# Optimization experiments

Hardware: AMD Instinct MI355X
Metric: run time of the kernel (lower is better)

## Reference

```python
import jax, jax.numpy as jnp
import numpy as np

TEMP = 1.0
EULER_GAMMA = 0.5772156649015329
BIG = 1.0e9


def setup_inputs() -> dict:
    key = jax.random.key(0)
    k = jax.random.split(key, 8)
    B, N, D, H = 32, 1024, 1024, 512  # batch, seq, d_model, hidden_size//2
    queries = jax.random.normal(k[0], (B, N, D), jnp.float32)
    queries_mask = jnp.ones((B, N), dtype=bool)
    W1 = jax.random.normal(k[1], (D, H), jnp.float32) * 0.02
    b1 = jnp.zeros((H,), jnp.float32)
    W2 = jax.random.normal(k[2], (H, 1), jnp.float32) * 0.02
    b2 = jnp.zeros((1,), jnp.float32)
    uniform_noise = jax.random.uniform(k[3], (B, N, 1), jnp.float32, 0.0, 1e-5)
    gumbel_noise = jax.random.gumbel(k[4], (B, N, 1), jnp.float32)
    return {"queries": queries, "queries_mask": queries_mask, "W1": W1, "b1": b1,
            "W2": W2, "b2": b2, "uniform_noise": uniform_noise,
            "gumbel_noise": gumbel_noise, "action_refinement": 1}


def reference(queries, queries_mask, W1, b1, W2, b2, uniform_noise, gumbel_noise, action_refinement):
    B, N, D = queries.shape
    # block0: Dense(H, relu) -> Dense(1); then softplus clamp + log + tiny uniform noise
    h = jax.nn.relu(jnp.einsum('bnd,dh->bnh', queries, W1) + b1)
    acts = jnp.einsum('bnh,ho->bno', h, W2) + b2                      # [B,N,1]
    acts = jnp.log(jnp.maximum(jax.nn.softplus(acts), 1e-5)) + uniform_noise
    acts = jnp.repeat(acts, action_refinement, axis=0)                # [BR,N,1]
    vmask = jnp.repeat(queries_mask[:, None, :].astype(jnp.float32), action_refinement, axis=0)  # [BR,1,N]
    n_valid = jnp.sum(vmask, axis=-1)                                 # [BR,1]
    mask_n1 = jnp.transpose(vmask, (0, 2, 1))                         # [BR,N,1]
    sqz_mask = mask_n1[..., 0]                                        # [BR,N]
    masked_acts = jnp.where(mask_n1 > 0, acts, -1e6)                  # [BR,N,1]
    perturb = masked_acts + gumbel_noise                              # [BR,N,1]
    # deterministic NeuralSort
    s = (jnp.exp(perturb) * mask_n1)[..., 0]                          # [BR,N]
    A = jnp.abs(s[:, :, None] - s[:, None, :])                        # [BR,N,N]
    Bmat = jnp.sum(A, axis=-1, keepdims=True)                         # A @ (1 1^T): row sums broadcast
    scaling = (N + 1 - 2 * (jnp.arange(N) + 1)).astype(jnp.float32)   # [N]
    C = s[:, :, None] * scaling[None, None, :]                        # [BR,N,N]
    P_hat = jnp.transpose(C - Bmat, (0, 2, 1)) - (1.0 - vmask) * BIG  # [BR,N,N]
    # greedy argmax permutation extraction (find_permu), vectorized over batch
    BR = P_hat.shape[0]
    def step(flag, row):                                              # row: [BR,N]
        tmp = row - flag * BIG
        idx = jnp.argmax(tmp, axis=-1)
        flag = jnp.maximum(flag, jax.nn.one_hot(idx, N, dtype=flag.dtype))
        return flag, idx
    _, idxs = jax.lax.scan(step, jnp.zeros((BR, N), jnp.float32), jnp.transpose(P_hat, (1, 0, 2)))
    chosen = jnp.transpose(idxs).astype(jnp.int32)                    # [BR,N]
    chosen = jnp.concatenate([jnp.zeros((BR, 1), jnp.int32), chosen[:, :-1]], axis=-1)
    id_permu = jnp.arange(N, dtype=jnp.int32)[None, :]
    permu = jnp.where(sqz_mask > 0, chosen, id_permu)                 # [BR,N]
    sample_permu = jax.nn.one_hot(permu, N, axis=-1, dtype=jnp.float32)
    # Plackett-Luce log-likelihood of sampled permutation
    exp_actis = jnp.exp(jnp.take_along_axis(masked_acts[..., 0], permu, axis=-1))
    rev_cumsum = jnp.cumsum(exp_actis[:, ::-1], axis=-1)[:, ::-1]
    eps = 1e-20
    log_nom = (jnp.log(exp_actis + eps) - jnp.log(rev_cumsum + eps)) * sqz_mask
    log_nom = jnp.sum(log_nom, axis=-1, keepdims=True)                # [BR,1]
    log_norm = jnp.zeros_like(log_nom)
    # KL term
    sqz_acts = acts[..., 0]
    kl1 = n_valid * (np.log(TEMP) - 1.0 + EULER_GAMMA * (1.0 / TEMP - 1.0))
    s1 = (1.0 / TEMP) * jnp.sum(sqz_acts * sqz_mask, axis=-1).reshape(-1, 1)
    s2 = jnp.sum(jnp.exp(-1.0 / TEMP * jnp.maximum(sqz_acts * sqz_mask, -20.0 * TEMP)), axis=-1).reshape(-1, 1) - (jnp.float32(N) - n_valid)
    kl = kl1 + s1 + s2 * jnp.exp(jax.lax.lgamma(jnp.float32(1.0 + 1.0 / TEMP)))
    return sample_permu, masked_acts[..., 0], kl, log_nom, log_norm
```

## Files before the change

### kernel.cpp

```cpp
#include <hip/hip_runtime.h>
#include <math.h>

#define BB 32
#define NN 1024
#define DD 1024
#define HH 512

#define OUT0_OFF 0
#define OUT1_OFF (BB * NN * NN)
#define OUT2_OFF (OUT1_OFF + BB * NN)
#define OUT3_OFF (OUT2_OFF + BB)
#define OUT4_OFF (OUT3_OFF + BB)

#define WS_ACTS 0
#define WS_W1T  131072
#define WS_RANK 1179648

typedef __attribute__((ext_vector_type(8))) short short8;
typedef __attribute__((ext_vector_type(4))) float floatx4;

__device__ inline unsigned int f2bf(float x) {
    unsigned int u = __builtin_bit_cast(unsigned int, x);
    return (u + 0x7FFFu + ((u >> 16) & 1u)) >> 16;
}

__device__ inline void gload_lds16(const void* g, void* l) {
    __builtin_amdgcn_global_load_lds(
        (const __attribute__((address_space(1))) unsigned int*)g,
        (__attribute__((address_space(3))) unsigned int*)l, 16, 0, 0);
}

__global__ __launch_bounds__(1024) void w1t_kernel(const float* __restrict__ W1,
                                                   unsigned short* __restrict__ W1T)
{
    __shared__ float T[32][33];
    const int tx = threadIdx.x, ty = threadIdx.y;
    const int d0 = blockIdx.x * 32, h0 = blockIdx.y * 32;
    T[ty][tx] = W1[(d0 + ty) * HH + h0 + tx];
    __syncthreads();
    W1T[(size_t)(h0 + ty) * DD + d0 + tx] = (unsigned short)f2bf(T[tx][ty]);
}

#define MT 128
__global__ __launch_bounds__(512, 2) void gemm_acts_kernel(
    const float* __restrict__ q, const unsigned short* __restrict__ W1T,
    const float* __restrict__ b1, const float* __restrict__ W2,
    const float* __restrict__ b2, const float* __restrict__ unoise,
    float* __restrict__ acts_ws, float* __restrict__ out1)
{
    __shared__ short As[2][MT * 32];
    __shared__ short Bs[2][HH * 32];
    __shared__ float red[MT][4];

    const int tid  = threadIdx.x;
    const int w    = tid >> 6;
    const int lane = tid & 63;
    const int c    = lane & 15;
    const int qd   = lane >> 4;
    const int wr   = (w >> 2) * 64;
    const int wc   = (w & 3) * 128;
    const int m0   = blockIdx.x * MT;

    floatx4 acc[8][4];
    #pragma unroll
    for (int tn = 0; tn < 8; ++tn)
        #pragma unroll
        for (int tm = 0; tm < 4; ++tm)
            acc[tn][tm] = (floatx4){0.f, 0.f, 0.f, 0.f};

    int boff[4];
    #pragma unroll
    for (int j = 0; j < 4; ++j) {
        int n  = (w * 4 + j) * 16 + (lane >> 2);
        int c0 = (lane & 3) * 16;
        int s  = (n >> 1) & 3;
        boff[j] = n * 2048 + (c0 ^ (s << 4));
    }
    const char* w1tb = (const char*)W1T;

    const int srow = tid >> 2, skp = tid & 3;
    const float* aptr = q + (size_t)(m0 + srow) * DD + skp * 8;
    const int asw = (skp * 16) ^ (((srow >> 1) & 3) << 4);

    int aoff[4], boffr[8];
    #pragma unroll
    for (int tm = 0; tm < 4; ++tm) {
        int r = wr + tm * 16 + c;
        aoff[tm] = r * 64 + ((qd * 16) ^ (((r >> 1) & 3) << 4));
    }
    #pragma unroll
    for (int tn = 0; tn < 8; ++tn) {
        int n = wc + tn * 16 + c;
        boffr[tn] = n * 64 + ((qd * 16) ^ (((n >> 1) & 3) << 4));
    }

    float4 a0, a1;

    #pragma unroll
    for (int j = 0; j < 4; ++j)
        gload_lds16(w1tb + boff[j], (char*)(&Bs[0][0]) + (w * 4 + j) * 1024);
    {
        const float4* ap = (const float4*)aptr;
        float4 v0 = ap[0], v1 = ap[1];
        uint4 pk;
        pk.x = f2bf(v0.x) | (f2bf(v0.y) << 16);
        pk.y = f2bf(v0.z) | (f2bf(v0.w) << 16);
        pk.z = f2bf(v1.x) | (f2bf(v1.y) << 16);
        pk.w = f2bf(v1.z) | (f2bf(v1.w) << 16);
        *(uint4*)((char*)(&As[0][0]) + srow * 64 + asw) = pk;
        const float4* ap1 = (const float4*)(aptr + 32);
        a0 = ap1[0]; a1 = ap1[1];
    }

    #pragma unroll 1
    for (int kk = 0; kk < 32; ++kk) {
        asm volatile("s_waitcnt vmcnt(0) lgkmcnt(0)" ::: "memory");
        __builtin_amdgcn_s_barrier();

        const int cur = kk & 1, nxt = cur ^ 1;
        if (kk < 31) {
            #pragma unroll
            for (int j = 0; j < 4; ++j)
                gload_lds16(w1tb + (boff[j] + (kk + 1) * 64),
                            (char*)(&Bs[nxt][0]) + (w * 4 + j) * 1024);
            uint4 pk;
            pk.x = f2bf(a0.x) | (f2bf(a0.y) << 16);
            pk.y = f2bf(a0.z) | (f2bf(a0.w) << 16);
            pk.z = f2bf(a1.x) | (f2bf(a1.y) << 16);
            pk.w = f2bf(a1.z) | (f2bf(a1.w) << 16);
            *(uint4*)((char*)(&As[nxt][0]) + srow * 64 + asw) = pk;
            const int ka = (kk < 30) ? kk + 2 : 31;
            const float4* ap = (const float4*)(aptr + ka * 32);
            a0 = ap[0]; a1 = ap[1];
        }
        __builtin_amdgcn_s_setprio(1);
        short8 af[4];
        #pragma unroll
        for (int tm = 0; tm < 4; ++tm)
            af[tm] = *(const short8*)((const char*)(&As[cur][0]) + aoff[tm]);
        #pragma unroll
        for (int tn = 0; tn < 8; ++tn) {
            short8 bf = *(const short8*)((const char*)(&Bs[cur][0]) + boffr[tn]);
            #pragma unroll
            for (int tm = 0; tm < 4; ++tm)
                acc[tn][tm] = __builtin_amdgcn_mfma_f32_16x16x32_bf16(
                    af[tm], bf, acc[tn][tm], 0, 0, 0);
        }
        __builtin_amdgcn_s_setprio(0);
    }

    float b1v[8], w2v[8];
    #pragma unroll
    for (int tn = 0; tn < 8; ++tn) {
        int col = wc + tn * 16 + c;
        b1v[tn] = b1[col];
        w2v[tn] = W2[col];
    }
    #pragma unroll
    for (int tm = 0; tm < 4; ++tm) {
        #pragma unroll
        for (int r = 0; r < 4; ++r) {
            float p = 0.f;
            #pragma unroll
            for (int tn = 0; tn < 8; ++tn) {
                float v = acc[tn][tm][r] + b1v[tn];
                p = fmaf(fmaxf(v, 0.f), w2v[tn], p);
            }
            p += __shfl_xor(p, 1);
            p += __shfl_xor(p, 2);
            p += __shfl_xor(p, 4);
            p += __shfl_xor(p, 8);
            if (c == 0) red[wr + tm * 16 + qd * 4 + r][w & 3] = p;
        }
    }
    __syncthreads();
    if (tid < MT) {
        float raw = red[tid][0] + red[tid][1] + red[tid][2] + red[tid][3] + b2[0];
        float sp = fmaxf(raw, 0.f) + log1pf(expf(-fabsf(raw)));
        int row = m0 + tid;
        float av = logf(fmaxf(sp, 1e-5f)) + unoise[row];
        acts_ws[row] = av;
        out1[row]    = av;
    }
}

__global__ __launch_bounds__(256) void zero_kernel(float4* __restrict__ p, int n4)
{
    int idx = blockIdx.x * blockDim.x + threadIdx.x;
    int stride = gridDim.x * blockDim.x;
    float4 z = make_float4(0.f, 0.f, 0.f, 0.f);
    for (int i = idx; i < n4; i += stride) p[i] = z;
}

__global__ __launch_bounds__(256) void rank_kernel(
    const float* __restrict__ acts_ws, const float* __restrict__ gumbel,
    int* __restrict__ rank)
{
    __shared__ float P[NN];
    const int b = blockIdx.x >> 2;
    const int chunk = blockIdx.x & 3;
    const int tid = threadIdx.x;
    #pragma unroll
    for (int r = 0; r < 4; ++r) {
        int j = r * 256 + tid;
        P[j] = acts_ws[b * NN + j] + gumbel[b * NN + j];
    }
    __syncthreads();
    const int i = chunk * 256 + tid;
    const float pert = P[i];
    int cnt = 0;
    const float4* P4 = (const float4*)P;
    for (int j4 = 0; j4 < NN / 4; ++j4) {
        float4 pv = P4[j4];
        int j = j4 * 4;
        cnt += (pv.x > pert) || (pv.x == pert && j + 0 < i);
        cnt += (pv.y > pert) || (pv.y == pert && j + 1 < i);
        cnt += (pv.z > pert) || (pv.z == pert && j + 2 < i);
        cnt += (pv.w > pert) || (pv.w == pert && j + 3 < i);
    }
    rank[b * NN + i] = cnt;
}

__global__ __launch_bounds__(1024) void permu_stats_kernel(
    const float* __restrict__ acts_ws, const int* __restrict__ rank,
    float* __restrict__ out0, float* __restrict__ out2,
    float* __restrict__ out3, float* __restrict__ out4)
{
    __shared__ float A[NN];
    __shared__ int   IDX[NN];
    __shared__ float WT[16];
    __shared__ float WSUF[17];
    __shared__ float P0[16], P1[16], P2[16];

    const int b = blockIdx.x;
    const int i = threadIdx.x;
    const int lane = i & 63;
    const int w = i >> 6;

    float a = acts_ws[b * NN + i];
    A[i] = a;
    IDX[rank[b * NN + i]] = i;
    __syncthreads();

    int perm = (i == 0) ? 0 : IDX[i - 1];
    out0[((size_t)b * NN + i) * NN + perm] = 1.0f;

    float e = expf(A[perm]);
    float s = e;
    #pragma unroll
    for (int off = 1; off < 64; off <<= 1) {
        float v = __shfl_down(s, off);
        if (lane + off < 64) s += v;
    }
    if (lane == 0) WT[w] = s;
    __syncthreads();
    if (w == 0) {
        float t = (lane < 16) ? WT[lane] : 0.f;
        #pragma unroll
        for (int off = 1; off < 16; off <<= 1) {
            float v = __shfl_down(t, off);
            if (lane + off < 16) t += v;
        }
        if (lane < 16) WSUF[lane] = t;
        if (lane == 0) WSUF[16] = 0.f;
    }
    __syncthreads();

    float S = s + WSUF[w + 1];
    float term = logf(e + 1e-20f) - logf(S + 1e-20f);

    float r0 = term, r1 = a, r2 = expf(-fmaxf(a, -20.f));
    #pragma unroll
    for (int off = 1; off < 64; off <<= 1) {
        r0 += __shfl_xor(r0, off);
        r1 += __shfl_xor(r1, off);
        r2 += __shfl_xor(r2, off);
    }
    if (lane == 0) { P0[w] = r0; P1[w] = r1; P2[w] = r2; }
    __syncthreads();
    if (i == 0) {
        float t0 = 0.f, t1 = 0.f, t2 = 0.f;
        #pragma unroll
        for (int k = 0; k < 16; ++k) { t0 += P0[k]; t1 += P1[k]; t2 += P2[k]; }
        out3[b] = t0;
        out2[b] = -(float)NN + t1 + t2;
        out4[b] = 0.f;
    }
}

extern "C" void kernel_launch(void* const* d_in, const int* in_sizes, int n_in,
                              void* d_out, int out_size, void* d_ws, size_t ws_size,
                              hipStream_t stream)
{
    const float* q      = (const float*)d_in[0];
    const float* W1     = (const float*)d_in[2];
    const float* b1     = (const float*)d_in[3];
    const float* W2     = (const float*)d_in[4];
    const float* b2     = (const float*)d_in[5];
    const float* unoise = (const float*)d_in[6];
    const float* gumbel = (const float*)d_in[7];

    float* out  = (float*)d_out;
    char*  ws   = (char*)d_ws;
    float*          acts = (float*)(ws + WS_ACTS);
    unsigned short* W1T  = (unsigned short*)(ws + WS_W1T);
    int*            rank = (int*)(ws + WS_RANK);

    w1t_kernel<<<dim3(32, 16), dim3(32, 32), 0, stream>>>(W1, W1T);
    gemm_acts_kernel<<<(BB * NN) / MT, 512, 0, stream>>>(q, W1T, b1, W2, b2,
                                                         unoise, acts,
                                                         out + OUT1_OFF);
    zero_kernel<<<8192, 256, 0, stream>>>((float4*)(out + OUT0_OFF),
                                          (BB * NN * NN) / 4);
    rank_kernel<<<BB * 4, 256, 0, stream>>>(acts, gumbel, rank);
    permu_stats_kernel<<<BB, 1024, 0, stream>>>(acts, rank,
                                                out + OUT0_OFF, out + OUT2_OFF,
                                                out + OUT3_OFF, out + OUT4_OFF);
}
```

Measured before the change: 310.9 us.

## Restructure GEMM to 64-row tiles with fine-grained vmcnt pipelining and 4 blocks/CU

Result: slower. 320.4 us (+3.0%).

```diff
diff --git a/kernel.cpp b/kernel.cpp
--- a/kernel.cpp
+++ b/kernel.cpp
@@ -41,29 +41,28 @@
     W1T[(size_t)(h0 + ty) * DD + d0 + tx] = (unsigned short)f2bf(T[tx][ty]);
 }
 
-#define MT 128
-__global__ __launch_bounds__(512, 2) void gemm_acts_kernel(
+#define MT 64
+#define SB() __builtin_amdgcn_sched_barrier(0)
+
+__global__ __launch_bounds__(512, 4) void gemm_acts_kernel(
     const float* __restrict__ q, const unsigned short* __restrict__ W1T,
     const float* __restrict__ b1, const float* __restrict__ W2,
     const float* __restrict__ b2, const float* __restrict__ unoise,
     float* __restrict__ acts_ws, float* __restrict__ out1)
 {
-    __shared__ short As[2][MT * 32];
+    __shared__ short As[2][MT * 64];
     __shared__ short Bs[2][HH * 32];
-    __shared__ float red[MT][4];
 
     const int tid  = threadIdx.x;
     const int w    = tid >> 6;
     const int lane = tid & 63;
     const int c    = lane & 15;
     const int qd   = lane >> 4;
-    const int wr   = (w >> 2) * 64;
-    const int wc   = (w & 3) * 128;
     const int m0   = blockIdx.x * MT;
 
-    floatx4 acc[8][4];
-    #pragma unroll
-    for (int tn = 0; tn < 8; ++tn)
+    floatx4 acc[4][4];
+    #pragma unroll
+    for (int tn = 0; tn < 4; ++tn)
         #pragma unroll
         for (int tm = 0; tm < 4; ++tm)
             acc[tn][tm] = (floatx4){0.f, 0.f, 0.f, 0.f};
@@ -78,91 +77,142 @@
     }
     const char* w1tb = (const char*)W1T;
 
-    const int srow = tid >> 2, skp = tid & 3;
-    const float* aptr = q + (size_t)(m0 + srow) * DD + skp * 8;
-    const int asw = (skp * 16) ^ (((srow >> 1) & 3) << 4);
-
-    int aoff[4], boffr[8];
+    const int arow = tid >> 3;
+    const int agrp = tid & 7;
+    const float* aptrA = q + (size_t)(m0 + arow) * DD + ((agrp ^ (arow & 7)) * 8);
+    const int adst = arow * 128 + agrp * 16;
+
+    int aoffA[4], aoffB[4], boffr[4];
     #pragma unroll
     for (int tm = 0; tm < 4; ++tm) {
-        int r = wr + tm * 16 + c;
-        aoff[tm] = r * 64 + ((qd * 16) ^ (((r >> 1) & 3) << 4));
-    }
-    #pragma unroll
-    for (int tn = 0; tn < 8; ++tn) {
-        int n = wc + tn * 16 + c;
+        int r = tm * 16 + c;
+        aoffA[tm] = r * 128 + 16 * ((qd)     ^ (r & 7));
+        aoffB[tm] = r * 128 + 16 * ((4 + qd) ^ (r & 7));
+    }
+    #pragma unroll
+    for (int tn = 0; tn < 4; ++tn) {
+        int n = w * 64 + tn * 16 + c;
         boffr[tn] = n * 64 + ((qd * 16) ^ (((n >> 1) & 3) << 4));
     }
 
     float4 a0, a1;
 
-    #pragma unroll
-    for (int j = 0; j < 4; ++j)
-        gload_lds16(w1tb + boff[j], (char*)(&Bs[0][0]) + (w * 4 + j) * 1024);
     {
-        const float4* ap = (const float4*)aptr;
-        float4 v0 = ap[0], v1 = ap[1];
+        float4 v0 = *(const float4*)(aptrA + 0);
+        float4 v1 = *(const float4*)(aptrA + 4);
         uint4 pk;
         pk.x = f2bf(v0.x) | (f2bf(v0.y) << 16);
         pk.y = f2bf(v0.z) | (f2bf(v0.w) << 16);
         pk.z = f2bf(v1.x) | (f2bf(v1.y) << 16);
         pk.w = f2bf(v1.z) | (f2bf(v1.w) << 16);
-        *(uint4*)((char*)(&As[0][0]) + srow * 64 + asw) = pk;
-        const float4* ap1 = (const float4*)(aptr + 32);
-        a0 = ap1[0]; a1 = ap1[1];
-    }
+        *(uint4*)((char*)(&As[0][0]) + adst) = pk;
+    }
+    SB();
+    #pragma unroll
+    for (int j = 0; j < 4; ++j)
+        gload_lds16(w1tb + boff[j], (char*)(&Bs[0][0]) + (w * 4 + j) * 1024);
+    SB();
+    a0 = *(const float4*)(aptrA + 64);
+    a1 = *(const float4*)(aptrA + 64 + 4);
+    SB();
+    #pragma unroll
+    for (int j = 0; j < 4; ++j)
+        gload_lds16(w1tb + (boff[j] + 64), (char*)(&Bs[1][0]) + (w * 4 + j) * 1024);
+    SB();
 
     #pragma unroll 1
-    for (int kk = 0; kk < 32; ++kk) {
-        asm volatile("s_waitcnt vmcnt(0) lgkmcnt(0)" ::: "memory");
+    for (int s = 0; s < 16; ++s) {
+        const int p = s & 1;
+        const char* asP = (const char*)(&As[p][0]);
+        char*       asN = (char*)(&As[p ^ 1][0]);
+
+        asm volatile("s_waitcnt lgkmcnt(0)" ::: "memory");
         __builtin_amdgcn_s_barrier();
-
-        const int cur = kk & 1, nxt = cur ^ 1;
-        if (kk < 31) {
+        asm volatile("s_waitcnt vmcnt(6)" ::: "memory");
+
+        {
+            short8 af[4];
+            #pragma unroll
+            for (int tm = 0; tm < 4; ++tm)
+                af[tm] = *(const short8*)(asP + aoffA[tm]);
+            __builtin_amdgcn_s_setprio(1);
+            #pragma unroll
+            for (int tn = 0; tn < 4; ++tn) {
+                short8 bf = *(const short8*)((const char*)(&Bs[0][0]) + boffr[tn]);
+                #pragma unroll
+                for (int tm = 0; tm < 4; ++tm)
+                    acc[tn][tm] = __builtin_amdgcn_mfma_f32_16x16x32_bf16(
+                        af[tm], bf, acc[tn][tm], 0, 0, 0);
+            }
+            __builtin_amdgcn_s_setprio(0);
+        }
+        SB();
+        if (s < 15) {
             #pragma unroll
             for (int j = 0; j < 4; ++j)
-                gload_lds16(w1tb + (boff[j] + (kk + 1) * 64),
-                            (char*)(&Bs[nxt][0]) + (w * 4 + j) * 1024);
-            uint4 pk;
-            pk.x = f2bf(a0.x) | (f2bf(a0.y) << 16);
-            pk.y = f2bf(a0.z) | (f2bf(a0.w) << 16);
-            pk.z = f2bf(a1.x) | (f2bf(a1.y) << 16);
-            pk.w = f2bf(a1.z) | (f2bf(a1.w) << 16);
-            *(uint4*)((char*)(&As[nxt][0]) + srow * 64 + asw) = pk;
-            const int ka = (kk < 30) ? kk + 2 : 31;
-            const float4* ap = (const float4*)(aptr + ka * 32);
-            a0 = ap[0]; a1 = ap[1];
-        }
-        __builtin_amdgcn_s_setprio(1);
-        short8 af[4];
-        #pragma unroll
-        for (int tm = 0; tm < 4; ++tm)
-            af[tm] = *(const short8*)((const char*)(&As[cur][0]) + aoff[tm]);
-        #pragma unroll
-        for (int tn = 0; tn < 8; ++tn) {
-            short8 bf = *(const short8*)((const char*)(&Bs[cur][0]) + boffr[tn]);
+                gload_lds16(w1tb + (boff[j] + (2 * s + 2) * 64),
+                            (char*)(&Bs[0][0]) + (w * 4 + j) * 1024);
+            SB();
+            asm volatile("s_waitcnt vmcnt(4)" ::: "memory");
+        } else {
+            asm volatile("s_waitcnt vmcnt(0)" ::: "memory");
+        }
+
+        {
+            short8 af[4];
             #pragma unroll
             for (int tm = 0; tm < 4; ++tm)
-                acc[tn][tm] = __builtin_amdgcn_mfma_f32_16x16x32_bf16(
-                    af[tm], bf, acc[tn][tm], 0, 0, 0);
-        }
-        __builtin_amdgcn_s_setprio(0);
-    }
-
-    float b1v[8], w2v[8];
-    #pragma unroll
-    for (int tn = 0; tn < 8; ++tn) {
-        int col = wc + tn * 16 + c;
+                af[tm] = *(const short8*)(asP + aoffB[tm]);
+            if (s < 15) {
+                uint4 pk;
+                pk.x = f2bf(a0.x) | (f2bf(a0.y) << 16);
+                pk.y = f2bf(a0.z) | (f2bf(a0.w) << 16);
+                pk.z = f2bf(a1.x) | (f2bf(a1.y) << 16);
+                pk.w = f2bf(a1.z) | (f2bf(a1.w) << 16);
+                *(uint4*)(asN + adst) = pk;
+                SB();
+                const int ka = (s < 14) ? s + 2 : 15;
+                a0 = *(const float4*)(aptrA + ka * 64);
+                a1 = *(const float4*)(aptrA + ka * 64 + 4);
+                SB();
+            }
+            __builtin_amdgcn_s_setprio(1);
+            #pragma unroll
+            for (int tn = 0; tn < 4; ++tn) {
+                short8 bf = *(const short8*)((const char*)(&Bs[1][0]) + boffr[tn]);
+                #pragma unroll
+                for (int tm = 0; tm < 4; ++tm)
+                    acc[tn][tm] = __builtin_amdgcn_mfma_f32_16x16x32_bf16(
+                        af[tm], bf, acc[tn][tm], 0, 0, 0);
+            }
+            __builtin_amdgcn_s_setprio(0);
+        }
+        SB();
+        if (s < 15) {
+            #pragma unroll
+            for (int j = 0; j < 4; ++j)
+                gload_lds16(w1tb + (boff[j] + (2 * s + 3) * 64),
+                            (char*)(&Bs[1][0]) + (w * 4 + j) * 1024);
+            SB();
+        }
+    }
+
+    float (*red)[8] = (float (*)[8])(&As[0][0]);
+    float b1v[4], w2v[4];
+    #pragma unroll
+    for (int tn = 0; tn < 4; ++tn) {
+        int col = w * 64 + tn * 16 + c;
         b1v[tn] = b1[col];
         w2v[tn] = W2[col];
     }
+    __syncthreads();
     #pragma unroll
     for (int tm = 0; tm < 4; ++tm) {
         #pragma unroll
         for (int r = 0; r < 4; ++r) {
             float p = 0.f;
             #pragma unroll
-            for (int tn = 0; tn < 8; ++tn) {
+            for (int tn = 0; tn < 4; ++tn) {
                 float v = acc[tn][tm][r] + b1v[tn];
                 p = fmaf(fmaxf(v, 0.f), w2v[tn], p);
             }
@@ -170,12 +220,13 @@
             p += __shfl_xor(p, 2);
             p += __shfl_xor(p, 4);
             p += __shfl_xor(p, 8);
-            if (c == 0) red[wr + tm * 16 + qd * 4 + r][w & 3] = p;
+            if (c == 0) red[tm * 16 + qd * 4 + r][w] = p;
         }
     }
     __syncthreads();
     if (tid < MT) {
-        float raw = red[tid][0] + red[tid][1] + red[tid][2] + red[tid][3] + b2[0];
+        float raw = red[tid][0] + red[tid][1] + red[tid][2] + red[tid][3] +
+                    red[tid][4] + red[tid][5] + red[tid][6] + red[tid][7] + b2[0];
         float sp = fmaxf(raw, 0.f) + log1pf(expf(-fabsf(raw)));
         int row = m0 + tid;
         float av = logf(fmaxf(sp, 1e-5f)) + unoise[row];
```

## Double GEMM K-tile to 64 with XOR swizzle and reuse LDS for reduction

Applied to the files above, without the earlier changes.

Result: no change. 309.5 us (-0.5%).

```diff
diff --git a/kernel.cpp b/kernel.cpp
--- a/kernel.cpp
+++ b/kernel.cpp
@@ -42,15 +42,16 @@
 }
 
 #define MT 128
+#define BK 64
+
 __global__ __launch_bounds__(512, 2) void gemm_acts_kernel(
     const float* __restrict__ q, const unsigned short* __restrict__ W1T,
     const float* __restrict__ b1, const float* __restrict__ W2,
     const float* __restrict__ b2, const float* __restrict__ unoise,
     float* __restrict__ acts_ws, float* __restrict__ out1)
 {
-    __shared__ short As[2][MT * 32];
-    __shared__ short Bs[2][HH * 32];
-    __shared__ float red[MT][4];
+    __shared__ short As[2][MT * BK];
+    __shared__ short Bs[2][HH * BK];
 
     const int tid  = threadIdx.x;
     const int w    = tid >> 6;
@@ -68,87 +69,115 @@
         for (int tm = 0; tm < 4; ++tm)
             acc[tn][tm] = (floatx4){0.f, 0.f, 0.f, 0.f};
 
-    int boff[4];
-    #pragma unroll
-    for (int j = 0; j < 4; ++j) {
-        int n  = (w * 4 + j) * 16 + (lane >> 2);
-        int c0 = (lane & 3) * 16;
-        int s  = (n >> 1) & 3;
-        boff[j] = n * 2048 + (c0 ^ (s << 4));
+    int boff[8];
+    #pragma unroll
+    for (int j = 0; j < 8; ++j) {
+        int n = w * 64 + j * 8 + (lane >> 3);
+        boff[j] = n * 2048 + (((lane & 7) ^ (lane >> 3)) << 4);
     }
     const char* w1tb = (const char*)W1T;
 
-    const int srow = tid >> 2, skp = tid & 3;
-    const float* aptr = q + (size_t)(m0 + srow) * DD + skp * 8;
-    const int asw = (skp * 16) ^ (((srow >> 1) & 3) << 4);
-
-    int aoff[4], boffr[8];
-    #pragma unroll
-    for (int tm = 0; tm < 4; ++tm) {
-        int r = wr + tm * 16 + c;
-        aoff[tm] = r * 64 + ((qd * 16) ^ (((r >> 1) & 3) << 4));
-    }
-    #pragma unroll
-    for (int tn = 0; tn < 8; ++tn) {
-        int n = wc + tn * 16 + c;
-        boffr[tn] = n * 64 + ((qd * 16) ^ (((n >> 1) & 3) << 4));
-    }
-
-    float4 a0, a1;
-
-    #pragma unroll
-    for (int j = 0; j < 4; ++j)
-        gload_lds16(w1tb + boff[j], (char*)(&Bs[0][0]) + (w * 4 + j) * 1024);
+    const int arow = tid >> 2;
+    const int u0   = (tid & 3) * 2;
+    const int s7   = arow & 7;
+    const float* ap0 = q + (size_t)(m0 + arow) * DD + ((u0       ^ s7) * 8);
+    const float* ap1 = q + (size_t)(m0 + arow) * DD + (((u0 + 1) ^ s7) * 8);
+    const int adst = arow * 128 + u0 * 16;
+
+    const int swz0 = ((qd)     ^ (c & 7)) << 4;
+    const int swz1 = ((4 + qd) ^ (c & 7)) << 4;
+
+    float4 a00, a01, a10, a11;
+
     {
-        const float4* ap = (const float4*)aptr;
-        float4 v0 = ap[0], v1 = ap[1];
-        uint4 pk;
-        pk.x = f2bf(v0.x) | (f2bf(v0.y) << 16);
-        pk.y = f2bf(v0.z) | (f2bf(v0.w) << 16);
-        pk.z = f2bf(v1.x) | (f2bf(v1.y) << 16);
-        pk.w = f2bf(v1.z) | (f2bf(v1.w) << 16);
-        *(uint4*)((char*)(&As[0][0]) + srow * 64 + asw) = pk;
-        const float4* ap1 = (const float4*)(aptr + 32);
-        a0 = ap1[0]; a1 = ap1[1];
-    }
+        float4 v00 = *(const float4*)(ap0);
+        float4 v01 = *(const float4*)(ap0 + 4);
+        float4 v10 = *(const float4*)(ap1);
+        float4 v11 = *(const float4*)(ap1 + 4);
+        uint4 p0, p1;
+        p0.x = f2bf(v00.x) | (f2bf(v00.y) << 16);
+        p0.y = f2bf(v00.z) | (f2bf(v00.w) << 16);
+        p0.z = f2bf(v01.x) | (f2bf(v01.y) << 16);
+        p0.w = f2bf(v01.z) | (f2bf(v01.w) << 16);
+        p1.x = f2bf(v10.x) | (f2bf(v10.y) << 16);
+        p1.y = f2bf(v10.z) | (f2bf(v10.w) << 16);
+        p1.z = f2bf(v11.x) | (f2bf(v11.y) << 16);
+        p1.w = f2bf(v11.z) | (f2bf(v11.w) << 16);
+        *(uint4*)((char*)(&As[0][0]) + adst)      = p0;
+        *(uint4*)((char*)(&As[0][0]) + adst + 16) = p1;
+    }
+    #pragma unroll
+    for (int j = 0; j < 8; ++j)
+        gload_lds16(w1tb + boff[j], (char*)(&Bs[0][0]) + w * 8192 + j * 1024);
+    a00 = *(const float4*)(ap0 + BK);
+    a01 = *(const float4*)(ap0 + BK + 4);
+    a10 = *(const float4*)(ap1 + BK);
+    a11 = *(const float4*)(ap1 + BK + 4);
 
     #pragma unroll 1
-    for (int kk = 0; kk < 32; ++kk) {
+    for (int kk = 0; kk < 16; ++kk) {
         asm volatile("s_waitcnt vmcnt(0) lgkmcnt(0)" ::: "memory");
         __builtin_amdgcn_s_barrier();
 
         const int cur = kk & 1, nxt = cur ^ 1;
-        if (kk < 31) {
-            #pragma unroll
-            for (int j = 0; j < 4; ++j)
-                gload_lds16(w1tb + (boff[j] + (kk + 1) * 64),
-                            (char*)(&Bs[nxt][0]) + (w * 4 + j) * 1024);
-            uint4 pk;
-            pk.x = f2bf(a0.x) | (f2bf(a0.y) << 16);
-            pk.y = f2bf(a0.z) | (f2bf(a0.w) << 16);
-            pk.z = f2bf(a1.x) | (f2bf(a1.y) << 16);
-            pk.w = f2bf(a1.z) | (f2bf(a1.w) << 16);
-            *(uint4*)((char*)(&As[nxt][0]) + srow * 64 + asw) = pk;
-            const int ka = (kk < 30) ? kk + 2 : 31;
-            const float4* ap = (const float4*)(aptr + ka * 32);
-            a0 = ap[0]; a1 = ap[1];
-        }
+        if (kk < 15) {
+            #pragma unroll
+            for (int j = 0; j < 8; ++j)
+                gload_lds16(w1tb + (boff[j] + (kk + 1) * 128),
+                            (char*)(&Bs[nxt][0]) + w * 8192 + j * 1024);
+            uint4 p0, p1;
+            p0.x = f2bf(a00.x) | (f2bf(a00.y) << 16);
+            p0.y = f2bf(a00.z) | (f2bf(a00.w) << 16);
+            p0.z = f2bf(a01.x) | (f2bf(a01.y) << 16);
+            p0.w = f2bf(a01.z) | (f2bf(a01.w) << 16);
+            p1.x = f2bf(a10.x) | (f2bf(a10.y) << 16);
+            p1.y = f2bf(a10.z) | (f2bf(a10.w) << 16);
+            p1.z = f2bf(a11.x) | (f2bf(a11.y) << 16);
+            p1.w = f2bf(a11.z) | (f2bf(a11.w) << 16);
+            *(uint4*)((char*)(&As[nxt][0]) + adst)      = p0;
+            *(uint4*)((char*)(&As[nxt][0]) + adst + 16) = p1;
+            const int ka = (kk < 14) ? kk + 2 : 15;
+            a00 = *(const float4*)(ap0 + ka * BK);
+            a01 = *(const float4*)(ap0 + ka * BK + 4);
+            a10 = *(const float4*)(ap1 + ka * BK);
+            a11 = *(const float4*)(ap1 + ka * BK + 4);
+        }
+
+        const char* asC = (const char*)(&As[cur][0]);
+        const char* bsC = (const char*)(&Bs[cur][0]);
         __builtin_amdgcn_s_setprio(1);
-        short8 af[4];
-        #pragma unroll
-        for (int tm = 0; tm < 4; ++tm)
-            af[tm] = *(const short8*)((const char*)(&As[cur][0]) + aoff[tm]);
-        #pragma unroll
-        for (int tn = 0; tn < 8; ++tn) {
-            short8 bf = *(const short8*)((const char*)(&Bs[cur][0]) + boffr[tn]);
+        {
+            short8 af[4];
             #pragma unroll
             for (int tm = 0; tm < 4; ++tm)
-                acc[tn][tm] = __builtin_amdgcn_mfma_f32_16x16x32_bf16(
-                    af[tm], bf, acc[tn][tm], 0, 0, 0);
+                af[tm] = *(const short8*)(asC + (wr + tm * 16 + c) * 128 + swz0);
+            #pragma unroll
+            for (int tn = 0; tn < 8; ++tn) {
+                short8 bf = *(const short8*)(bsC + (wc + tn * 16 + c) * 128 + swz0);
+                #pragma unroll
+                for (int tm = 0; tm < 4; ++tm)
+                    acc[tn][tm] = __builtin_amdgcn_mfma_f32_16x16x32_bf16(
+                        af[tm], bf, acc[tn][tm], 0, 0, 0);
+            }
+        }
+        {
+            short8 af[4];
+            #pragma unroll
+            for (int tm = 0; tm < 4; ++tm)
+                af[tm] = *(const short8*)(asC + (wr + tm * 16 + c) * 128 + swz1);
+            #pragma unroll
+            for (int tn = 0; tn < 8; ++tn) {
+                short8 bf = *(const short8*)(bsC + (wc + tn * 16 + c) * 128 + swz1);
+                #pragma unroll
+                for (int tm = 0; tm < 4; ++tm)
+                    acc[tn][tm] = __builtin_amdgcn_mfma_f32_16x16x32_bf16(
+                        af[tm], bf, acc[tn][tm], 0, 0, 0);
+            }
         }
         __builtin_amdgcn_s_setprio(0);
     }
 
+    float (*red)[4] = (float (*)[4])(&As[0][0]);
     float b1v[8], w2v[8];
     #pragma unroll
     for (int tn = 0; tn < 8; ++tn) {
```
